# Kernel optimization log

Hardware: AMD Instinct MI355X
Metric: run time of the kernel (lower is better)

## Reference

```python
import jax, jax.numpy as jnp
import numpy as np

N_NODES = 65536
N_EDGES = 262144
N_GRAPHS = 2048
NF = 16   # num_node_features
EF = 6    # num_edge_features
H1, H2, H3 = 32, 16, 8  # conv1 out, conv2 out, lin1 out


def _lin_init(key, fan_in, fan_out):
    kw, kb = jax.random.split(key)
    s = 1.0 / np.sqrt(fan_in)
    w = jax.random.uniform(kw, (fan_in, fan_out), minval=-s, maxval=s, dtype=jnp.float32)
    b = jax.random.uniform(kb, (fan_out,), minval=-s, maxval=s, dtype=jnp.float32)
    return w, b


def setup_inputs() -> dict:
    key = jax.random.key(0)
    ks = jax.random.split(key, 16)
    inp = {}
    inp["x_p"] = jax.random.normal(ks[0], (N_NODES, NF), dtype=jnp.float32)
    inp["x_d"] = jax.random.normal(ks[1], (4, NF), dtype=jnp.float32)  # unused by forward
    inp["edge_attr_p"] = jax.random.uniform(ks[2], (N_EDGES, EF), dtype=jnp.float32)
    inp["edge_attr_d"] = jax.random.uniform(ks[3], (4, EF), dtype=jnp.float32)  # unused
    inp["edge_index_p"] = jax.random.randint(ks[4], (2, N_EDGES), 0, N_NODES, dtype=jnp.int32)
    inp["x_p_batch"] = jnp.sort(jax.random.randint(ks[5], (N_NODES,), 0, N_GRAPHS, dtype=jnp.int32))
    # conv1: NNConv(NF, 32); edge nn: Linear(EF,16) -> ReLU -> Linear(16, NF*32)
    inp["nn1_w1"], inp["nn1_b1"] = _lin_init(ks[6], EF, 16)
    inp["nn1_w2"], inp["nn1_b2"] = _lin_init(ks[7], 16, NF * H1)
    inp["root1"] = _lin_init(ks[8], NF, H1)[0]
    inp["bias1"] = jnp.zeros((H1,), dtype=jnp.float32)
    # conv2: NNConv(32, 16); edge nn: Linear(EF,16) -> ReLU -> Linear(16, 32*16)
    inp["nn2_w1"], inp["nn2_b1"] = _lin_init(ks[9], EF, 16)
    inp["nn2_w2"], inp["nn2_b2"] = _lin_init(ks[10], 16, H1 * H2)
    inp["root2"] = _lin_init(ks[11], H1, H2)[0]
    inp["bias2"] = jnp.zeros((H2,), dtype=jnp.float32)
    # attention pooling gate: Linear(NF,NF) -> ReLU -> Linear(NF,1)
    inp["gate_w1"], inp["gate_b1"] = _lin_init(ks[12], NF, NF)
    inp["gate_w2"], inp["gate_b2"] = _lin_init(ks[13], NF, 1)
    # head: Linear(16+16, 8) -> Linear(8, 1)  (attention=True)
    inp["lin1_w"], inp["lin1_b"] = _lin_init(ks[14], H2 + NF, H3)
    inp["lin2_w"], inp["lin2_b"] = _lin_init(ks[15], H3, 1)
    return inp


def _nnconv(x, edge_attr, src, dst, w1, b1, w2, b2, root, bias, in_c, out_c, n_nodes):
    # per-edge dynamic weight matrix Theta(e) : [E, in_c, out_c]
    h = jax.nn.relu(edge_attr @ w1 + b1) @ w2 + b2
    w_dyn = h.reshape(-1, in_c, out_c)
    msg = jnp.einsum('ei,eio->eo', x[src], w_dyn)          # [E, out_c]
    agg = jax.ops.segment_sum(msg, dst, num_segments=n_nodes)  # scatter-add
    return agg + x @ root + bias


def _attention_pool(x, batch, gw1, gb1, gw2, gb2, n_graphs):
    g = (jax.nn.relu(x @ gw1 + gb1) @ gw2 + gb2)[:, 0]     # [N] gate logits
    m = jax.ops.segment_max(g, batch, num_segments=n_graphs)
    e = jnp.exp(g - m[batch])
    s = jax.ops.segment_sum(e, batch, num_segments=n_graphs)
    alpha = e / s[batch]                                    # per-graph softmax
    return jax.ops.segment_sum(alpha[:, None] * x, batch, num_segments=n_graphs)


def _mean_pool(x, batch, n_graphs):
    s = jax.ops.segment_sum(x, batch, num_segments=n_graphs)
    cnt = jax.ops.segment_sum(jnp.ones((x.shape[0],), x.dtype), batch, num_segments=n_graphs)
    return s / jnp.maximum(cnt, 1.0)[:, None]


def reference(x_p, x_d, edge_attr_p, edge_attr_d, edge_index_p, x_p_batch,
              nn1_w1, nn1_b1, nn1_w2, nn1_b2, root1, bias1,
              nn2_w1, nn2_b1, nn2_w2, nn2_b2, root2, bias2,
              gate_w1, gate_b1, gate_w2, gate_b2,
              lin1_w, lin1_b, lin2_w, lin2_b):
    src, dst = edge_index_p[0], edge_index_p[1]
    # attention pooling on raw node features (attention=True)
    x_att = _attention_pool(x_p, x_p_batch, gate_w1, gate_b1, gate_w2, gate_b2, N_GRAPHS)
    # two NNConv layers with ReLU
    h = jax.nn.relu(_nnconv(x_p, edge_attr_p, src, dst, nn1_w1, nn1_b1, nn1_w2, nn1_b2,
                            root1, bias1, NF, H1, N_NODES))
    h = jax.nn.relu(_nnconv(h, edge_attr_p, src, dst, nn2_w1, nn2_b1, nn2_w2, nn2_b2,
                            root2, bias2, H1, H2, N_NODES))
    g = _mean_pool(h, x_p_batch, N_GRAPHS)                  # [B, 16]
    g = jnp.concatenate([g, x_att], axis=1)                 # [B, 32]
    # dropout p=0.5 is identity in eval mode
    g = g @ lin1_w + lin1_b
    out = g @ lin2_w + lin2_b                               # [B, 1]
    return out
```

## Files before the change

kernel.cpp:

```cpp
#include <hip/hip_runtime.h>

#define NN 65536
#define NE 262144
#define NG 2048

typedef __attribute__((ext_vector_type(16))) float f32x16;
typedef __attribute__((ext_vector_type(4)))  float f32x4;
typedef __attribute__((ext_vector_type(8)))  __bf16 bf16x8;

__device__ inline unsigned pack2(float a, float b) {
    return __builtin_amdgcn_perm(__float_as_uint(b), __float_as_uint(a), 0x07060302u);
}
__device__ inline float lof(float p) {
    return p - __uint_as_float(__float_as_uint(p) & 0xffff0000u);
}
__device__ inline bf16x8 asb(uint4 u) { return __builtin_bit_cast(bf16x8, u); }

__global__ __launch_bounds__(256) void k_setup(
    const int* __restrict__ batch,
    const float* __restrict__ w2a, const float* __restrict__ b2a,
    const float* __restrict__ w2b, const float* __restrict__ b2c,
    int* __restrict__ cnt, int* __restrict__ cur, int* __restrict__ goffs,
    unsigned* __restrict__ f1, unsigned* __restrict__ f2)
{
    int t = blockIdx.x * 256 + threadIdx.x;
    if (t < NN) { cnt[t] = 0; cur[t] = 0; }
    if (t <= NG) {
        int lo = 0, hi = NN;
        while (lo < hi) {
            int mid = (lo + hi) >> 1;
            if (batch[mid] < t) lo = mid + 1; else hi = mid;
        }
        goffs[t] = lo;
    }
    if (t < 17408) {
        int c = t / 8704;
        int r = t - c * 8704;
        int d = r & 3;
        int l = (r >> 2) & 63;
        int tt = (r >> 8) & 1;
        int s = r >> 9;
        if (c == 0) {
            int n = l & 31, g = l >> 5;
            int j0 = 2*d;
            int c0 = (g*8 + j0)*32 + n;
            int c1 = c0 + 32;
            float a = (s < 16) ? w2a[s*512 + c0] : b2a[c0];
            float b = (s < 16) ? w2a[s*512 + c1] : b2a[c1];
            f1[r] = tt ? pack2(lof(a), lof(b)) : pack2(a, b);
        } else {
            int n = l & 15, g = l >> 4;
            int j0 = 2*d;
            int c0 = (g*8 + j0)*16 + n;
            int c1 = c0 + 16;
            float a = (s < 16) ? w2b[s*512 + c0] : b2c[c0];
            float b = (s < 16) ? w2b[s*512 + c1] : b2c[c1];
            f2[r] = tt ? pack2(lof(a), lof(b)) : pack2(a, b);
        }
    }
}

__global__ __launch_bounds__(64) void k_gateatt(const float* __restrict__ x,
    const float* __restrict__ gw1, const float* __restrict__ gb1,
    const float* __restrict__ gw2, const float* __restrict__ gb2,
    const int* __restrict__ goffs, float* __restrict__ x_att)
{
    __shared__ float sw[256];
    __shared__ float sb[16];
    __shared__ float sw2[16];
    __shared__ float sb2;
    __shared__ float gb[1024];
    const int g = blockIdx.x;
    const int lane = threadIdx.x;
    for (int i = lane; i < 256; i += 64) sw[i] = gw1[i];
    if (lane < 16) { sb[lane] = gb1[lane]; sw2[lane] = gw2[lane]; }
    if (lane == 0) sb2 = gb2[0];
    const int s = goffs[g], e = goffs[g + 1];
    const int cnt = e - s;
    if (cnt <= 0) {
        if (lane < 16) x_att[g*16 + lane] = 0.f;
        return;
    }
    const int cap = cnt < 1024 ? cnt : 1024;
    __syncthreads();
    for (int ii = lane; ii < cap; ii += 64) {
        const float4* xp = (const float4*)(x + (size_t)(s + ii) * 16);
        float xv[16];
#pragma unroll
        for (int i = 0; i < 4; ++i) {
            float4 tt = xp[i];
            xv[4*i] = tt.x; xv[4*i+1] = tt.y; xv[4*i+2] = tt.z; xv[4*i+3] = tt.w;
        }
        float gv = sb2;
#pragma unroll
        for (int j = 0; j < 16; ++j) {
            float a = sb[j];
#pragma unroll
            for (int i = 0; i < 16; ++i) a += xv[i] * sw[i*16 + j];
            gv += fmaxf(a, 0.f) * sw2[j];
        }
        gb[ii] = gv;
    }
    __syncthreads();
    float m = -1e30f;
    for (int ii = lane; ii < cap; ii += 64) m = fmaxf(m, gb[ii]);
#pragma unroll
    for (int d = 32; d; d >>= 1) m = fmaxf(m, __shfl_xor(m, d));
    float sum = 0.f;
    for (int ii = lane; ii < cap; ii += 64) {
        float ev = expf(gb[ii] - m);
        gb[ii] = ev;
        sum += ev;
    }
#pragma unroll
    for (int d = 32; d; d >>= 1) sum += __shfl_xor(sum, d);
    const float inv = 1.f / sum;
    __syncthreads();
    const int f = lane & 15, sub = lane >> 4;
    float acc = 0.f;
    for (int ii = sub; ii < cap; ii += 4)
        acc += gb[ii] * inv * x[(size_t)(s + ii)*16 + f];
    acc += __shfl_xor(acc, 16);
    acc += __shfl_xor(acc, 32);
    if (lane < 16) x_att[g*16 + f] = acc;
}

__global__ __launch_bounds__(256) void k_hist(const int* __restrict__ ei, int* __restrict__ cnt)
{
    int e = blockIdx.x * 256 + threadIdx.x;
    if (e >= NE) return;
    atomicAdd(&cnt[ei[NE + e]], 1);
}

__global__ __launch_bounds__(256) void k_scan_blk(const int* __restrict__ cnt,
    int* __restrict__ offs, int* __restrict__ bsum)
{
    __shared__ int s[256];
    int t = threadIdx.x, b = blockIdx.x;
    int v = cnt[b*256 + t];
    s[t] = v;
    __syncthreads();
#pragma unroll
    for (int d = 1; d < 256; d <<= 1) {
        int add = (t >= d) ? s[t - d] : 0;
        __syncthreads();
        s[t] += add;
        __syncthreads();
    }
    offs[b*256 + t] = s[t] - v;
    if (t == 255) bsum[b] = s[255];
}

__global__ __launch_bounds__(256) void k_scan_top(const int* __restrict__ bsum,
    int* __restrict__ boff)
{
    __shared__ int s[256];
    int t = threadIdx.x;
    int v = bsum[t];
    s[t] = v;
    __syncthreads();
#pragma unroll
    for (int d = 1; d < 256; d <<= 1) {
        int add = (t >= d) ? s[t - d] : 0;
        __syncthreads();
        s[t] += add;
        __syncthreads();
    }
    boff[t] = s[t] - v;
}

__global__ __launch_bounds__(256) void k_scan_add(int* __restrict__ offs,
    const int* __restrict__ boff)
{
    int i = blockIdx.x * 256 + threadIdx.x;
    if (i == 0) offs[NN] = NE;
    if (i >= NN) return;
    offs[i] += boff[i >> 8];
}

__global__ __launch_bounds__(256) void k_scatter(const int* __restrict__ ei,
    const int* __restrict__ offs, int* __restrict__ cur,
    int* __restrict__ eperm, int* __restrict__ esrc)
{
    int e = blockIdx.x * 256 + threadIdx.x;
    if (e >= NE) return;
    int d = ei[NE + e];
    int pos = offs[d] + atomicAdd(&cur[d], 1);
    eperm[pos] = e;
    esrc[pos] = ei[e];
}

__global__ __launch_bounds__(256) void k_conv1(
    const float* __restrict__ x, const float* __restrict__ ea,
    const int* __restrict__ eperm, const int* __restrict__ esrc,
    const float* __restrict__ w1, const float* __restrict__ b1,
    const unsigned* __restrict__ bfrag, float* __restrict__ msg)
{
    const int tid  = threadIdx.x;
    const int lane = tid & 63;
    const int wid  = tid >> 6;
    const int m    = lane & 31;
    const int g    = lane >> 5;
    const uint4* bf4 = (const uint4*)bfrag;

    const int tile = blockIdx.x*4 + wid;
    const int p    = tile*32 + m;
    const int src  = esrc[p];
    const int e    = eperm[p];

    float xs[8];
    {
        const float4* xp = (const float4*)(x + (size_t)src*16 + g*8);
        float4 aa = xp[0], bb = xp[1];
        xs[0]=aa.x; xs[1]=aa.y; xs[2]=aa.z; xs[3]=aa.w;
        xs[4]=bb.x; xs[5]=bb.y; xs[6]=bb.z; xs[7]=bb.w;
    }
    float h[17];
    {
        const float2 e01 = *(const float2*)(ea + (size_t)e*6);
        const float2 e23 = *(const float2*)(ea + (size_t)e*6 + 2);
        const float2 e45 = *(const float2*)(ea + (size_t)e*6 + 4);
        const float a0=e01.x, a1=e01.y, a2=e23.x, a3=e23.y, a4=e45.x, a5=e45.y;
#pragma unroll
        for (int j = 0; j < 16; ++j) {
            float c = b1[j];
            c += a0*w1[0*16+j]; c += a1*w1[1*16+j]; c += a2*w1[2*16+j];
            c += a3*w1[3*16+j]; c += a4*w1[4*16+j]; c += a5*w1[5*16+j];
            h[j] = fmaxf(c, 0.f);
        }
        h[16] = 1.f;
    }

    f32x16 acc0 = {}, acc1 = {};
#pragma unroll
    for (int s = 0; s < 17; ++s) {
        const float hs = h[s];
        float p0 = hs*xs[0], p1 = hs*xs[1], p2 = hs*xs[2], p3 = hs*xs[3];
        float p4 = hs*xs[4], p5 = hs*xs[5], p6 = hs*xs[6], p7 = hs*xs[7];
        uint4 uh = { pack2(p0,p1), pack2(p2,p3), pack2(p4,p5), pack2(p6,p7) };
        uint4 ul = { pack2(lof(p0),lof(p1)), pack2(lof(p2),lof(p3)),
                     pack2(lof(p4),lof(p5)), pack2(lof(p6),lof(p7)) };
        uint4 wh = bf4[(s*2+0)*64 + lane];
        uint4 wl = bf4[(s*2+1)*64 + lane];
        if (s & 1) {
            acc1 = __builtin_amdgcn_mfma_f32_32x32x16_bf16(asb(uh), asb(wh), acc1, 0, 0, 0);
            acc1 = __builtin_amdgcn_mfma_f32_32x32x16_bf16(asb(uh), asb(wl), acc1, 0, 0, 0);
            acc1 = __builtin_amdgcn_mfma_f32_32x32x16_bf16(asb(ul), asb(wh), acc1, 0, 0, 0);
        } else {
            acc0 = __builtin_amdgcn_mfma_f32_32x32x16_bf16(asb(uh), asb(wh), acc0, 0, 0, 0);
            acc0 = __builtin_amdgcn_mfma_f32_32x32x16_bf16(asb(uh), asb(wl), acc0, 0, 0, 0);
            acc0 = __builtin_amdgcn_mfma_f32_32x32x16_bf16(asb(ul), asb(wh), acc0, 0, 0, 0);
        }
    }

    float* mbase = msg + (size_t)tile*32*32;
    const int rb = g*4;
#pragma unroll
    for (int r = 0; r < 16; ++r) {
        int mr = (r&3) + 8*(r>>2) + rb;
        mbase[(size_t)mr*32 + m] = acc0[r] + acc1[r];
    }
}

__global__ __launch_bounds__(256) void k_conv2(
    const float* __restrict__ x, const float* __restrict__ ea,
    const int* __restrict__ eperm, const int* __restrict__ esrc,
    const float* __restrict__ w1, const float* __restrict__ b1,
    const unsigned* __restrict__ bfrag, float* __restrict__ msg)
{
    const int tid  = threadIdx.x;
    const int lane = tid & 63;
    const int wid  = tid >> 6;
    const int m    = lane & 15;
    const int g    = lane >> 4;
    const uint4* bf4 = (const uint4*)bfrag;

    const int tile = blockIdx.x*4 + wid;
    const int p    = tile*16 + m;
    const int src  = esrc[p];
    const int e    = eperm[p];

    float xs[8];
    {
        const float4* xp = (const float4*)(x + (size_t)src*32 + g*8);
        float4 aa = xp[0], bb = xp[1];
        xs[0]=aa.x; xs[1]=aa.y; xs[2]=aa.z; xs[3]=aa.w;
        xs[4]=bb.x; xs[5]=bb.y; xs[6]=bb.z; xs[7]=bb.w;
    }
    float h[17];
    {
        const float2 e01 = *(const float2*)(ea + (size_t)e*6);
        const float2 e23 = *(const float2*)(ea + (size_t)e*6 + 2);
        const float2 e45 = *(const float2*)(ea + (size_t)e*6 + 4);
        const float a0=e01.x, a1=e01.y, a2=e23.x, a3=e23.y, a4=e45.x, a5=e45.y;
#pragma unroll
        for (int j = 0; j < 16; ++j) {
            float c = b1[j];
            c += a0*w1[0*16+j]; c += a1*w1[1*16+j]; c += a2*w1[2*16+j];
            c += a3*w1[3*16+j]; c += a4*w1[4*16+j]; c += a5*w1[5*16+j];
            h[j] = fmaxf(c, 0.f);
        }
        h[16] = 1.f;
    }

    f32x4 acc0 = {}, acc1 = {};
#pragma unroll
    for (int s = 0; s < 17; ++s) {
        const float hs = h[s];
        float p0 = hs*xs[0], p1 = hs*xs[1], p2 = hs*xs[2], p3 = hs*xs[3];
        float p4 = hs*xs[4], p5 = hs*xs[5], p6 = hs*xs[6], p7 = hs*xs[7];
        uint4 uh = { pack2(p0,p1), pack2(p2,p3), pack2(p4,p5), pack2(p6,p7) };
        uint4 ul = { pack2(lof(p0),lof(p1)), pack2(lof(p2),lof(p3)),
                     pack2(lof(p4),lof(p5)), pack2(lof(p6),lof(p7)) };
        uint4 wh = bf4[(s*2+0)*64 + lane];
        uint4 wl = bf4[(s*2+1)*64 + lane];
        if (s & 1) {
            acc1 = __builtin_amdgcn_mfma_f32_16x16x32_bf16(asb(uh), asb(wh), acc1, 0, 0, 0);
            acc1 = __builtin_amdgcn_mfma_f32_16x16x32_bf16(asb(uh), asb(wl), acc1, 0, 0, 0);
            acc1 = __builtin_amdgcn_mfma_f32_16x16x32_bf16(asb(ul), asb(wh), acc1, 0, 0, 0);
        } else {
            acc0 = __builtin_amdgcn_mfma_f32_16x16x32_bf16(asb(uh), asb(wh), acc0, 0, 0, 0);
            acc0 = __builtin_amdgcn_mfma_f32_16x16x32_bf16(asb(uh), asb(wl), acc0, 0, 0, 0);
            acc0 = __builtin_amdgcn_mfma_f32_16x16x32_bf16(asb(ul), asb(wh), acc0, 0, 0, 0);
        }
    }

    float* mbase = msg + (size_t)tile*16*16;
#pragma unroll
    for (int r = 0; r < 4; ++r) {
        int mr = g*4 + r;
        mbase[(size_t)mr*16 + m] = acc0[r] + acc1[r];
    }
}

__global__ __launch_bounds__(256) void k_reduce1(
    const float* __restrict__ msg, const int* __restrict__ offs,
    const float* __restrict__ x, const float* __restrict__ root,
    const float* __restrict__ bias, float* __restrict__ h1)
{
    __shared__ float s_r[512];
    __shared__ float s_b[32];
    int tid = threadIdx.x;
    for (int i = tid; i < 512; i += 256) s_r[i] = root[i];
    if (tid < 32) s_b[tid] = bias[tid];
    __syncthreads();
    int gid = blockIdx.x * 256 + tid;
    int n = gid >> 3, q = gid & 7;
    int s = offs[n], e = offs[n + 1];
    float4 acc = make_float4(s_b[4*q], s_b[4*q+1], s_b[4*q+2], s_b[4*q+3]);
    const float4* s_r4 = (const float4*)s_r;
    const float* xp = x + (size_t)n * 16;
#pragma unroll
    for (int i = 0; i < 16; ++i) {
        float xi = xp[i];
        float4 w = s_r4[i*8 + q];
        acc.x += xi*w.x; acc.y += xi*w.y; acc.z += xi*w.z; acc.w += xi*w.w;
    }
    for (int p = s; p < e; ++p) {
        float4 mr = ((const float4*)(msg + (size_t)p * 32))[q];
        acc.x += mr.x; acc.y += mr.y; acc.z += mr.z; acc.w += mr.w;
    }
    acc.x = fmaxf(acc.x, 0.f); acc.y = fmaxf(acc.y, 0.f);
    acc.z = fmaxf(acc.z, 0.f); acc.w = fmaxf(acc.w, 0.f);
    ((float4*)(h1 + (size_t)n * 32))[q] = acc;
}

__global__ __launch_bounds__(256) void k_reduce2(
    const float* __restrict__ msg, const int* __restrict__ offs,
    const float* __restrict__ h1, const float* __restrict__ root,
    const float* __restrict__ bias, float* __restrict__ h2)
{
    __shared__ float s_r[512];
    __shared__ float s_b[16];
    int tid = threadIdx.x;
    for (int i = tid; i < 512; i += 256) s_r[i] = root[i];
    if (tid < 16) s_b[tid] = bias[tid];
    __syncthreads();
    int gid = blockIdx.x * 256 + tid;
    int n = gid >> 2, q = gid & 3;
    int s = offs[n], e = offs[n + 1];
    float4 acc = make_float4(s_b[4*q], s_b[4*q+1], s_b[4*q+2], s_b[4*q+3]);
    const float4* s_r4 = (const float4*)s_r;
    const float* xp = h1 + (size_t)n * 32;
#pragma unroll
    for (int i = 0; i < 32; ++i) {
        float xi = xp[i];
        float4 w = s_r4[i*4 + q];
        acc.x += xi*w.x; acc.y += xi*w.y; acc.z += xi*w.z; acc.w += xi*w.w;
    }
    for (int p = s; p < e; ++p) {
        float4 mr = ((const float4*)(msg + (size_t)p * 16))[q];
        acc.x += mr.x; acc.y += mr.y; acc.z += mr.z; acc.w += mr.w;
    }
    acc.x = fmaxf(acc.x, 0.f); acc.y = fmaxf(acc.y, 0.f);
    acc.z = fmaxf(acc.z, 0.f); acc.w = fmaxf(acc.w, 0.f);
    ((float4*)(h2 + (size_t)n * 16))[q] = acc;
}

__global__ __launch_bounds__(64) void k_head(
    const float* __restrict__ h2, const float* __restrict__ x_att,
    const int* __restrict__ goffs,
    const float* __restrict__ l1w, const float* __restrict__ l1b,
    const float* __restrict__ l2w, const float* __restrict__ l2b,
    float* __restrict__ out)
{
    int g = blockIdx.x;
    int lane = threadIdx.x;
    int s = goffs[g], e = goffs[g + 1];
    __shared__ float v[32];
    __shared__ float hmid[8];
    int f = lane & 15, sub = lane >> 4;
    float acc = 0.f;
    for (int i = s + sub; i < e; i += 4) acc += h2[(size_t)i*16 + f];
    acc += __shfl_xor(acc, 16);
    acc += __shfl_xor(acc, 32);
    float cnt = fmaxf((float)(e - s), 1.0f);
    if (lane < 16) {
        v[lane]      = acc / cnt;
        v[16 + lane] = x_att[g*16 + lane];
    }
    __syncthreads();
    if (lane < 8) {
        float a = l1b[lane];
#pragma unroll
        for (int i = 0; i < 32; ++i) a += v[i] * l1w[i*8 + lane];
        hmid[lane] = a;
    }
    __syncthreads();
    if (lane == 0) {
        float a = l2b[0];
#pragma unroll
        for (int j = 0; j < 8; ++j) a += hmid[j] * l2w[j];
        out[g] = a;
    }
}

extern "C" void kernel_launch(void* const* d_in, const int* in_sizes, int n_in,
                              void* d_out, int out_size, void* d_ws, size_t ws_size,
                              hipStream_t stream) {
    const float* x_p    = (const float*)d_in[0];
    const float* ea_p   = (const float*)d_in[2];
    const int*   ei     = (const int*)d_in[4];
    const int*   batch  = (const int*)d_in[5];
    const float* nn1_w1 = (const float*)d_in[6];
    const float* nn1_b1 = (const float*)d_in[7];
    const float* nn1_w2 = (const float*)d_in[8];
    const float* nn1_b2 = (const float*)d_in[9];
    const float* root1  = (const float*)d_in[10];
    const float* bias1  = (const float*)d_in[11];
    const float* nn2_w1 = (const float*)d_in[12];
    const float* nn2_b1 = (const float*)d_in[13];
    const float* nn2_w2 = (const float*)d_in[14];
    const float* nn2_b2 = (const float*)d_in[15];
    const float* root2  = (const float*)d_in[16];
    const float* bias2  = (const float*)d_in[17];
    const float* gw1    = (const float*)d_in[18];
    const float* gb1    = (const float*)d_in[19];
    const float* gw2    = (const float*)d_in[20];
    const float* gb2    = (const float*)d_in[21];
    const float* l1w    = (const float*)d_in[22];
    const float* l1b    = (const float*)d_in[23];
    const float* l2w    = (const float*)d_in[24];
    const float* l2b    = (const float*)d_in[25];

    float*    h1     = (float*)d_ws;
    float*    h2     = h1 + (size_t)NN * 32;
    float*    x_att  = h2 + (size_t)NN * 16;
    int*      goffs  = (int*)(x_att + (size_t)NG * 16);
    int*      offs   = goffs + 2052;
    int*      cnt    = offs + 65540;
    int*      cur    = cnt + NN;
    int*      bsum   = cur + NN;
    int*      boff   = bsum + 256;
    int*      eperm  = boff + 256;
    int*      esrc   = eperm + NE;
    unsigned* bfrag1 = (unsigned*)(esrc + NE);
    unsigned* bfrag2 = bfrag1 + 8704;
    float*    msg    = (float*)(bfrag2 + 8704);

    k_setup<<<512, 256, 0, stream>>>(batch, nn1_w2, nn1_b2, nn2_w2, nn2_b2,
                                     cnt, cur, goffs, bfrag1, bfrag2);

    k_gateatt<<<NG, 64, 0, stream>>>(x_p, gw1, gb1, gw2, gb2, goffs, x_att);

    k_hist<<<NE/256, 256, 0, stream>>>(ei, cnt);
    k_scan_blk<<<NN/256, 256, 0, stream>>>(cnt, offs, bsum);
    k_scan_top<<<1, 256, 0, stream>>>(bsum, boff);
    k_scan_add<<<NN/256, 256, 0, stream>>>(offs, boff);
    k_scatter<<<NE/256, 256, 0, stream>>>(ei, offs, cur, eperm, esrc);

    k_conv1<<<2048, 256, 0, stream>>>(x_p, ea_p, eperm, esrc, nn1_w1, nn1_b1, bfrag1, msg);
    k_reduce1<<<NN*8/256, 256, 0, stream>>>(msg, offs, x_p, root1, bias1, h1);

    k_conv2<<<4096, 256, 0, stream>>>(h1, ea_p, eperm, esrc, nn2_w1, nn2_b1, bfrag2, msg);
    k_reduce2<<<NN*4/256, 256, 0, stream>>>(msg, offs, h1, root2, bias2, h2);

    k_head<<<NG, 64, 0, stream>>>(h2, x_att, goffs, l1w, l1b, l2w, l2b, (float*)d_out);
}
```

Before: 138.8 us.

## Factor per-edge hidden scale out of conv2 MFMA and transpose output via LDS

Conv2 now splits x into bf16 hi/lo once and computes W_s·x per hidden unit with MFMA, then scales each result by h[s] in fp32 and accumulates. Before, it rebuilt h·x products and repacked them for every hidden unit. This removes the per-step multiply and pack work. The MFMA operands are swapped so each edge's 16 outputs come out transposed; they are staged through per-wave LDS and written back as coalesced float4 stores. This adds an LDS round trip and a fresh accumulator chain per step, which serializes the MFMAs.

```diff
diff --git a/kernel.cpp b/kernel.cpp
--- a/kernel.cpp
+++ b/kernel.cpp
@@ -268,6 +268,7 @@
     const float* __restrict__ w1, const float* __restrict__ b1,
     const unsigned* __restrict__ bfrag, float* __restrict__ msg)
 {
+    __shared__ float lt[4][16*21];
     const int tid  = threadIdx.x;
     const int lane = tid & 63;
     const int wid  = tid >> 6;
@@ -280,12 +281,14 @@
     const int src  = esrc[p];
     const int e    = eperm[p];
 
-    float xs[8];
+    uint4 xh, xl;
     {
         const float4* xp = (const float4*)(x + (size_t)src*32 + g*8);
         float4 aa = xp[0], bb = xp[1];
-        xs[0]=aa.x; xs[1]=aa.y; xs[2]=aa.z; xs[3]=aa.w;
-        xs[4]=bb.x; xs[5]=bb.y; xs[6]=bb.z; xs[7]=bb.w;
+        float v0=aa.x, v1=aa.y, v2=aa.z, v3=aa.w, v4=bb.x, v5=bb.y, v6=bb.z, v7=bb.w;
+        xh = (uint4){ pack2(v0,v1), pack2(v2,v3), pack2(v4,v5), pack2(v6,v7) };
+        xl = (uint4){ pack2(lof(v0),lof(v1)), pack2(lof(v2),lof(v3)),
+                      pack2(lof(v4),lof(v5)), pack2(lof(v6),lof(v7)) };
     }
     float h[17];
     {
@@ -303,34 +306,32 @@
         h[16] = 1.f;
     }
 
-    f32x4 acc0 = {}, acc1 = {};
+    f32x4 macc = {};
 #pragma unroll
     for (int s = 0; s < 17; ++s) {
-        const float hs = h[s];
-        float p0 = hs*xs[0], p1 = hs*xs[1], p2 = hs*xs[2], p3 = hs*xs[3];
-        float p4 = hs*xs[4], p5 = hs*xs[5], p6 = hs*xs[6], p7 = hs*xs[7];
-        uint4 uh = { pack2(p0,p1), pack2(p2,p3), pack2(p4,p5), pack2(p6,p7) };
-        uint4 ul = { pack2(lof(p0),lof(p1)), pack2(lof(p2),lof(p3)),
-                     pack2(lof(p4),lof(p5)), pack2(lof(p6),lof(p7)) };
         uint4 wh = bf4[(s*2+0)*64 + lane];
         uint4 wl = bf4[(s*2+1)*64 + lane];
-        if (s & 1) {
-            acc1 = __builtin_amdgcn_mfma_f32_16x16x32_bf16(asb(uh), asb(wh), acc1, 0, 0, 0);
-            acc1 = __builtin_amdgcn_mfma_f32_16x16x32_bf16(asb(uh), asb(wl), acc1, 0, 0, 0);
-            acc1 = __builtin_amdgcn_mfma_f32_16x16x32_bf16(asb(ul), asb(wh), acc1, 0, 0, 0);
-        } else {
-            acc0 = __builtin_amdgcn_mfma_f32_16x16x32_bf16(asb(uh), asb(wh), acc0, 0, 0, 0);
-            acc0 = __builtin_amdgcn_mfma_f32_16x16x32_bf16(asb(uh), asb(wl), acc0, 0, 0, 0);
-            acc0 = __builtin_amdgcn_mfma_f32_16x16x32_bf16(asb(ul), asb(wh), acc0, 0, 0, 0);
-        }
-    }
-
-    float* mbase = msg + (size_t)tile*16*16;
-#pragma unroll
-    for (int r = 0; r < 4; ++r) {
-        int mr = g*4 + r;
-        mbase[(size_t)mr*16 + m] = acc0[r] + acc1[r];
-    }
+        f32x4 t = {};
+        t = __builtin_amdgcn_mfma_f32_16x16x32_bf16(asb(wh), asb(xh), t, 0, 0, 0);
+        t = __builtin_amdgcn_mfma_f32_16x16x32_bf16(asb(wl), asb(xh), t, 0, 0, 0);
+        t = __builtin_amdgcn_mfma_f32_16x16x32_bf16(asb(wh), asb(xl), t, 0, 0, 0);
+        const float hs = h[s];
+        macc.x += hs*t.x; macc.y += hs*t.y; macc.z += hs*t.z; macc.w += hs*t.w;
+    }
+
+    float* lw = lt[wid];
+    lw[m*21 + g*4 + 0] = macc.x;
+    lw[m*21 + g*4 + 1] = macc.y;
+    lw[m*21 + g*4 + 2] = macc.z;
+    lw[m*21 + g*4 + 3] = macc.w;
+    asm volatile("s_waitcnt lgkmcnt(0)" ::: "memory");
+    const int rrow = lane >> 2, fq = lane & 3;
+    float o0 = lw[rrow*21 + fq*4 + 0];
+    float o1 = lw[rrow*21 + fq*4 + 1];
+    float o2 = lw[rrow*21 + fq*4 + 2];
+    float o3 = lw[rrow*21 + fq*4 + 3];
+    float4* mb = (float4*)(msg + (size_t)tile*256);
+    mb[rrow*4 + fq] = make_float4(o0, o1, o2, o3);
 }
 
 __global__ __launch_bounds__(256) void k_reduce1(
```

New measurement: 138.3 us. Within noise of the previous version (-0.4%).
